# Optimization experiments

Measured on AMD Instinct MI355X. Metric: run time of the kernel, lower is better.

The kernel has to match this reference:

```python
import jax, jax.numpy as jnp
import numpy as np

B = 4096      # batch (tokens)
D_IN = 1024   # input_size_expert
D_HID = 4096  # hidden_size_expert
D_OUT = 1024  # output_size
E = 8         # num_experts


def setup_inputs() -> dict:
    key = jax.random.key(0)
    ks = jax.random.split(key, 9)
    s = lambda fan_in: 1.0 / np.sqrt(fan_in)
    x_expert = jax.random.normal(ks[0], (B, D_IN), dtype=jnp.float32)
    # per-expert weights stacked on leading E axis
    W1 = jax.random.uniform(ks[1], (E, D_IN, D_HID), jnp.float32, -s(D_IN), s(D_IN))
    b1 = jax.random.uniform(ks[2], (E, D_HID), jnp.float32, -s(D_IN), s(D_IN))
    W2 = jax.random.uniform(ks[3], (E, D_HID, D_OUT), jnp.float32, -s(D_HID), s(D_HID))
    b2 = jax.random.uniform(ks[4], (E, D_OUT), jnp.float32, -s(D_HID), s(D_HID))
    # gating network (input_size_gating = input_size_expert, hidden_size_gating = hidden_size_expert)
    Wg1 = jax.random.uniform(ks[5], (D_IN, D_HID), jnp.float32, -s(D_IN), s(D_IN))
    bg1 = jax.random.uniform(ks[6], (D_HID,), jnp.float32, -s(D_IN), s(D_IN))
    Wg2 = jax.random.uniform(ks[7], (D_HID, E), jnp.float32, -s(D_HID), s(D_HID))
    bg2 = jax.random.uniform(ks[8], (E,), jnp.float32, -s(D_HID), s(D_HID))
    return {"x_expert": x_expert, "W1": W1, "b1": b1, "W2": W2, "b2": b2,
            "Wg1": Wg1, "bg1": bg1, "Wg2": Wg2, "bg2": bg2}


def reference(x_expert, W1, b1, W2, b2, Wg1, bg1, Wg2, bg2):
    # gating: MLP + softmax over experts -> [B, E]
    g = jax.nn.relu(x_expert @ Wg1 + bg1)
    gate = jax.nn.softmax(g @ Wg2 + bg2, axis=1)
    # all experts as one batched GEMM: [B, E, D_HID]
    h = jax.nn.relu(jnp.einsum('bi,eih->beh', x_expert, W1) + b1)
    expert_out = jnp.einsum('beh,eho->beo', h, W2) + b2  # [B, E, D_OUT]
    # gate-weighted sum over experts
    return jnp.einsum('be,beo->bo', gate, expert_out)
```

## Files before the change

kernel.cpp:

```cpp
#include <hip/hip_runtime.h>
#include <stdint.h>

typedef __bf16 bf16;
typedef __attribute__((ext_vector_type(8))) __bf16 bf16x8;
typedef __attribute__((ext_vector_type(4))) float f32x4;
typedef unsigned short u16;
typedef unsigned int u32;

#define B_TOK 4096
#define D_IN  1024
#define D_HID 4096
#define D_OUT 1024
#define NE    8
#define KTOT  (NE * D_HID)

#define AS1 __attribute__((address_space(1)))
#define AS3 __attribute__((address_space(3)))

__device__ __forceinline__ u16 f2bf(float f) {
  u32 u = __float_as_uint(f);
  return (u16)((u + 0x7FFFu + ((u >> 16) & 1u)) >> 16);
}
__device__ __forceinline__ u32 pack2(float a, float b) {
  return (u32)f2bf(a) | ((u32)f2bf(b) << 16);
}

__global__ __launch_bounds__(256) void cvt_bf16_kernel(const float* __restrict__ in,
                                                       u32* __restrict__ out, long n) {
  long i = ((long)blockIdx.x * 256 + threadIdx.x) * 8;
  if (i >= n) return;
  const float4* pf = (const float4*)(in + i);
  float4 f0 = pf[0], f1 = pf[1];
  uint4 o = make_uint4(pack2(f0.x, f0.y), pack2(f0.z, f0.w),
                       pack2(f1.x, f1.y), pack2(f1.z, f1.w));
  *(uint4*)(out + i / 2) = o;
}

__global__ __launch_bounds__(256) void transpose_bf16_kernel(const float* __restrict__ in,
                                                             u16* __restrict__ out,
                                                             int R, int C) {
  __shared__ u16 tileT[64][68];
  const size_t bo = (size_t)blockIdx.z * R * C;
  const int c0 = blockIdx.x * 64, r0 = blockIdx.y * 64;
  const int tid = threadIdx.x;
  const int lr = tid >> 4;
  const int lc = (tid & 15) * 4;
#pragma unroll
  for (int p = 0; p < 4; ++p) {
    const int r = p * 16 + lr;
    const float4 v = *(const float4*)(in + bo + (size_t)(r0 + r) * C + c0 + lc);
    tileT[lc + 0][r] = f2bf(v.x);
    tileT[lc + 1][r] = f2bf(v.y);
    tileT[lc + 2][r] = f2bf(v.z);
    tileT[lc + 3][r] = f2bf(v.w);
  }
  __syncthreads();
  const int oc  = tid >> 3;
  const int och = (tid & 7) * 8;
#pragma unroll
  for (int p = 0; p < 2; ++p) {
    const int c = p * 32 + oc;
    bf16x8 v = *(const bf16x8*)(&tileT[c][och]);
    *(bf16x8*)(out + bo + (size_t)(c0 + c) * R + r0 + och) = v;
  }
}

template<int MODE>
__global__ __launch_bounds__(512, 2) void gemm_mfma256(
    const bf16* __restrict__ A,
    const bf16* __restrict__ Bt,
    const float* __restrict__ bias,
    const float* __restrict__ gate,
    void* __restrict__ Cptr,
    int K, long ldB, long kOffB, long ldC, int kIters, int eArg)
{
  __shared__ __align__(16) bf16 smem[65536];

  const int tid  = threadIdx.x;
  const int wave = tid >> 6;
  const int lane = tid & 63;
  const int quad = lane >> 4;
  const int l16  = lane & 15;
  const int wr = (wave >> 2) * 128;
  const int wc = (wave & 3) * 64;

  const int m0 = blockIdx.x * 256;
  const int n0 = blockIdx.y * 256;

  int expert = 0;
  long cColOff = 0;
  const bf16* Bp = Bt;
  const float* biasP = bias;
  if (MODE == 1) {
    if (gridDim.z > 1) { expert = blockIdx.z; cColOff = (long)expert * D_HID; }
    else               { expert = eArg; }
    Bp = Bt + (size_t)expert * D_HID * (size_t)ldB;
    biasP = bias + (size_t)expert * D_HID;
  }
  const int nt = kIters;
  const long kBase = (MODE == 2) ? (long)blockIdx.z * nt * 64 : 0;

  const int sRow = lane >> 3;
  const int sCol = ((lane & 7) ^ sRow) * 8;

  const bf16* aSrc = A  + (size_t)(m0 + wave * 8 + sRow) * K   + kBase + sCol;
  const bf16* bSrc = Bp + (size_t)(n0 + wave * 8 + sRow) * ldB + kOffB + kBase + sCol;
  const int dOff = (wave * 8) * 64;

  f32x4 acc[8][4];
#pragma unroll
  for (int i = 0; i < 8; ++i)
#pragma unroll
    for (int j = 0; j < 4; ++j)
      acc[i][j] = (f32x4){0.f, 0.f, 0.f, 0.f};

#define GLL(tt, bb) do { \
    bf16* dstA = smem + (bb) * 32768 + dOff; \
    bf16* dstB = dstA + 16384; \
    const bf16* srcA = aSrc + (size_t)(tt) * 64; \
    const bf16* srcB = bSrc + (size_t)(tt) * 64; \
    _Pragma("unroll") \
    for (int g_ = 0; g_ < 4; ++g_) { \
      __builtin_amdgcn_global_load_lds((AS1 void*)(srcA + (size_t)g_ * 64 * K), \
                                       (AS3 void*)(dstA + g_ * 64 * 64), 16, 0, 0); \
      __builtin_amdgcn_global_load_lds((AS1 void*)(srcB + (size_t)g_ * 64 * ldB), \
                                       (AS3 void*)(dstB + g_ * 64 * 64), 16, 0, 0); \
    } \
  } while (0)

  GLL(0, 0);

  for (int t = 0; t < nt; ++t) {
    const bf16* Ab = smem + (t & 1) * 32768;
    const bf16* Bb = Ab + 16384;
    asm volatile("s_waitcnt vmcnt(0)" ::: "memory");
    __builtin_amdgcn_s_barrier();
    if (t + 1 < nt) GLL(t + 1, (t + 1) & 1);
#pragma unroll
    for (int kh = 0; kh < 2; ++kh) {
      const int sw = (((kh << 2) + quad) ^ (l16 & 7)) << 3;
      bf16x8 bv[4], av[8];
#pragma unroll
      for (int j = 0; j < 4; ++j)
        bv[j] = *(const bf16x8*)(Bb + (wc + j * 16 + l16) * 64 + sw);
#pragma unroll
      for (int i = 0; i < 8; ++i)
        av[i] = *(const bf16x8*)(Ab + (wr + i * 16 + l16) * 64 + sw);
      __builtin_amdgcn_s_setprio(1);
#pragma unroll
      for (int i = 0; i < 8; ++i)
#pragma unroll
        for (int j = 0; j < 4; ++j)
          acc[i][j] = __builtin_amdgcn_mfma_f32_16x16x32_bf16(av[i], bv[j], acc[i][j], 0, 0, 0);
      __builtin_amdgcn_s_setprio(0);
    }
  }
#undef GLL

  if (MODE <= 1) {
    const int SL = 72;
    u16* slab = (u16*)smem + wave * (16 * SL);
    u16* C = (u16*)Cptr;
    float bv[4];
#pragma unroll
    for (int j = 0; j < 4; ++j) bv[j] = biasP[n0 + wc + j * 16 + l16];
#pragma unroll
    for (int i = 0; i < 8; ++i) {
#pragma unroll
      for (int r = 0; r < 4; ++r) {
        const int lrow = quad * 4 + r;
        float sc = 1.0f;
        if (MODE == 1) sc = gate[(size_t)(m0 + wr + i * 16 + lrow) * NE + expert];
#pragma unroll
        for (int j = 0; j < 4; ++j) {
          float v = fmaxf(acc[i][j][r] + bv[j], 0.0f) * sc;
          slab[lrow * SL + j * 16 + l16] = f2bf(v);
        }
      }
      const int rrow = lane & 15;
      const int c0c  = lane >> 4;
      bf16x8 v0 = *(const bf16x8*)(slab + rrow * SL + c0c * 8);
      bf16x8 v1 = *(const bf16x8*)(slab + rrow * SL + (c0c + 4) * 8);
      u16* orow = C + (size_t)(m0 + wr + i * 16 + rrow) * ldC + cColOff + n0 + wc;
      *(bf16x8*)(orow + c0c * 8)       = v0;
      *(bf16x8*)(orow + (c0c + 4) * 8) = v1;
    }
  } else {
    float* C = (float*)Cptr;
#pragma unroll
    for (int i = 0; i < 8; ++i) {
#pragma unroll
      for (int r = 0; r < 4; ++r) {
        const int row = m0 + wr + i * 16 + quad * 4 + r;
        float* crow = C + (size_t)row * ldC + n0 + wc + l16;
#pragma unroll
        for (int j = 0; j < 4; ++j)
          atomicAdd(crow + j * 16, acc[i][j][r]);
      }
    }
  }
}

__global__ __launch_bounds__(256) void gate_softmax_kernel(const bf16* __restrict__ g,
                                                           const float* __restrict__ Wg2,
                                                           const float* __restrict__ bg2,
                                                           float* __restrict__ gate) {
  const int wave = threadIdx.x >> 6, lane = threadIdx.x & 63;
  const int row = blockIdx.x * 4 + wave;
  const bf16* gr = g + (size_t)row * D_HID;
  float acc[NE];
#pragma unroll
  for (int e = 0; e < NE; ++e) acc[e] = 0.f;
  for (int k = lane; k < D_HID; k += 64) {
    const float gv = (float)gr[k];
    const float* w = Wg2 + (size_t)k * NE;
#pragma unroll
    for (int e = 0; e < NE; ++e) acc[e] += gv * w[e];
  }
#pragma unroll
  for (int e = 0; e < NE; ++e) {
    float v = acc[e];
#pragma unroll
    for (int off = 32; off > 0; off >>= 1) v += __shfl_down(v, off);
    acc[e] = v;
  }
  if (lane == 0) {
    float mx = -3.4e38f;
#pragma unroll
    for (int e = 0; e < NE; ++e) { acc[e] += bg2[e]; mx = fmaxf(mx, acc[e]); }
    float s = 0.f;
#pragma unroll
    for (int e = 0; e < NE; ++e) { acc[e] = __expf(acc[e] - mx); s += acc[e]; }
    const float inv = 1.f / s;
#pragma unroll
    for (int e = 0; e < NE; ++e) gate[(size_t)row * NE + e] = acc[e] * inv;
  }
}

__global__ __launch_bounds__(256) void gate_bias_kernel(const float* __restrict__ gate,
                                                        const float* __restrict__ b2,
                                                        float* __restrict__ out) {
  const int idx = blockIdx.x * 256 + threadIdx.x;
  const int b = idx >> 8;
  const int o = (idx & 255) * 4;
  float4 v = {0.f, 0.f, 0.f, 0.f};
#pragma unroll
  for (int e = 0; e < NE; ++e) {
    const float gv = gate[(size_t)b * NE + e];
    const float4 bb = *(const float4*)(b2 + (size_t)e * D_OUT + o);
    v.x += gv * bb.x; v.y += gv * bb.y; v.z += gv * bb.z; v.w += gv * bb.w;
  }
  *(float4*)(out + (size_t)b * D_OUT + o) = v;
}

extern "C" void kernel_launch(void* const* d_in, const int* in_sizes, int n_in,
                              void* d_out, int out_size, void* d_ws, size_t ws_size,
                              hipStream_t stream) {
  const float* x   = (const float*)d_in[0];
  const float* W1  = (const float*)d_in[1];
  const float* b1  = (const float*)d_in[2];
  const float* W2  = (const float*)d_in[3];
  const float* b2  = (const float*)d_in[4];
  const float* Wg1 = (const float*)d_in[5];
  const float* bg1 = (const float*)d_in[6];
  const float* Wg2 = (const float*)d_in[7];
  const float* bg2 = (const float*)d_in[8];
  float* out = (float*)d_out;

  char* p = (char*)d_ws;
  bf16* xb   = (bf16*)p; p += (size_t)B_TOK * D_IN * 2;
  bf16* Wg1t = (bf16*)p; p += (size_t)D_HID * D_IN * 2;
  bf16* W1t  = (bf16*)p; p += (size_t)NE * D_HID * D_IN * 2;
  bf16* W2t  = (bf16*)p; p += (size_t)D_OUT * KTOT * 2;
  bf16* g    = (bf16*)p; p += (size_t)B_TOK * D_HID * 2;
  float* gate= (float*)p; p += (size_t)B_TOK * NE * 4;
  bf16* hs   = (bf16*)p;
  const size_t fixed = (size_t)(p - (char*)d_ws);
  const bool big = ws_size >= fixed + (size_t)B_TOK * KTOT * 2;

  cvt_bf16_kernel<<<(B_TOK * D_IN / 8 + 255) / 256, 256, 0, stream>>>(x, (u32*)xb, (long)B_TOK * D_IN);
  transpose_bf16_kernel<<<dim3(D_HID / 64, D_IN / 64, 1), 256, 0, stream>>>(Wg1, (u16*)Wg1t, D_IN, D_HID);
  transpose_bf16_kernel<<<dim3(D_HID / 64, D_IN / 64, NE), 256, 0, stream>>>(W1, (u16*)W1t, D_IN, D_HID);
  transpose_bf16_kernel<<<dim3(D_OUT / 64, KTOT / 64, 1), 256, 0, stream>>>(W2, (u16*)W2t, KTOT, D_OUT);
  gemm_mfma256<0><<<dim3(16, 16, 1), 512, 0, stream>>>(xb, Wg1t, bg1, nullptr, g,
                                                       D_IN, (long)D_IN, 0L, (long)D_HID, D_IN / 64, 0);
  gate_softmax_kernel<<<B_TOK / 4, 256, 0, stream>>>(g, Wg2, bg2, gate);
  gate_bias_kernel<<<B_TOK * D_OUT / 4 / 256, 256, 0, stream>>>(gate, b2, out);

  if (big) {
    gemm_mfma256<1><<<dim3(16, 16, NE), 512, 0, stream>>>(xb, W1t, b1, gate, hs,
                                                          D_IN, (long)D_IN, 0L, (long)KTOT, D_IN / 64, 0);
    gemm_mfma256<2><<<dim3(16, 4, 8), 512, 0, stream>>>(hs, W2t, nullptr, nullptr, out,
                                                        KTOT, (long)KTOT, 0L, (long)D_OUT, KTOT / 8 / 64, 0);
  } else {
    for (int e = 0; e < NE; ++e) {
      gemm_mfma256<1><<<dim3(16, 16, 1), 512, 0, stream>>>(xb, W1t, b1, gate, hs,
                                                           D_IN, (long)D_IN, 0L, (long)D_HID, D_IN / 64, e);
      gemm_mfma256<2><<<dim3(16, 4, 2), 512, 0, stream>>>(hs, W2t, nullptr, nullptr, out,
                                                          D_HID, (long)KTOT, (long)e * D_HID, (long)D_OUT,
                                                          D_HID / 2 / 64, e);
    }
  }
}
```

Baseline: 1.006 ms.

## Use 256x128 GEMM tiles with triple-buffered LDS and interleaved prefetch

Shrinks the GEMM block tile from 256x256 to 256x128 and switches from double to triple buffering in LDS, issuing prefetch two tiles ahead. The prefetch loads are split so that half go out before the first MFMA half-step and half after it, with a partial vmcnt wait. Grids are doubled along N, and the split-K factor for the second expert GEMM drops from 8 to 4. This aims at better latency hiding and more blocks in flight, at the cost of lower arithmetic intensity per block and more A-tile reloads.

Result: no change. 1.016 ms (+1.1%).

```diff
diff --git a/kernel.cpp b/kernel.cpp
--- a/kernel.cpp
+++ b/kernel.cpp
@@ -74,7 +74,7 @@
     void* __restrict__ Cptr,
     int K, long ldB, long kOffB, long ldC, int kIters, int eArg)
 {
-  __shared__ __align__(16) bf16 smem[65536];
+  __shared__ __align__(16) bf16 smem[3 * 24576];
 
   const int tid  = threadIdx.x;
   const int wave = tid >> 6;
@@ -82,10 +82,10 @@
   const int quad = lane >> 4;
   const int l16  = lane & 15;
   const int wr = (wave >> 2) * 128;
-  const int wc = (wave & 3) * 64;
+  const int wc = (wave & 3) * 32;
 
   const int m0 = blockIdx.x * 256;
-  const int n0 = blockIdx.y * 256;
+  const int n0 = blockIdx.y * 128;
 
   int expert = 0;
   long cColOff = 0;
@@ -105,65 +105,76 @@
 
   const bf16* aSrc = A  + (size_t)(m0 + wave * 8 + sRow) * K   + kBase + sCol;
   const bf16* bSrc = Bp + (size_t)(n0 + wave * 8 + sRow) * ldB + kOffB + kBase + sCol;
-  const int dOff = (wave * 8) * 64;
-
-  f32x4 acc[8][4];
+
+  f32x4 acc[8][2];
 #pragma unroll
   for (int i = 0; i < 8; ++i)
 #pragma unroll
-    for (int j = 0; j < 4; ++j)
+    for (int j = 0; j < 2; ++j)
       acc[i][j] = (f32x4){0.f, 0.f, 0.f, 0.f};
 
-#define GLL(tt, bb) do { \
-    bf16* dstA = smem + (bb) * 32768 + dOff; \
-    bf16* dstB = dstA + 16384; \
-    const bf16* srcA = aSrc + (size_t)(tt) * 64; \
-    const bf16* srcB = bSrc + (size_t)(tt) * 64; \
-    _Pragma("unroll") \
-    for (int g_ = 0; g_ < 4; ++g_) { \
-      __builtin_amdgcn_global_load_lds((AS1 void*)(srcA + (size_t)g_ * 64 * K), \
-                                       (AS3 void*)(dstA + g_ * 64 * 64), 16, 0, 0); \
-      __builtin_amdgcn_global_load_lds((AS1 void*)(srcB + (size_t)g_ * 64 * ldB), \
-                                       (AS3 void*)(dstB + g_ * 64 * 64), 16, 0, 0); \
+#define GST(tt, bb, s) do { \
+    if ((s) < 4) { \
+      __builtin_amdgcn_global_load_lds( \
+        (AS1 void*)(aSrc + (size_t)(tt) * 64 + (size_t)(s) * 64 * K), \
+        (AS3 void*)(smem + (bb) * 24576 + (s) * 4096 + wave * 512), 16, 0, 0); \
+    } else { \
+      __builtin_amdgcn_global_load_lds( \
+        (AS1 void*)(bSrc + (size_t)(tt) * 64 + (size_t)((s) - 4) * 64 * ldB), \
+        (AS3 void*)(smem + (bb) * 24576 + 16384 + ((s) - 4) * 4096 + wave * 512), 16, 0, 0); \
     } \
   } while (0)
 
-  GLL(0, 0);
-
-  for (int t = 0; t < nt; ++t) {
-    const bf16* Ab = smem + (t & 1) * 32768;
-    const bf16* Bb = Ab + 16384;
-    asm volatile("s_waitcnt vmcnt(0)" ::: "memory");
-    __builtin_amdgcn_s_barrier();
-    if (t + 1 < nt) GLL(t + 1, (t + 1) & 1);
-#pragma unroll
-    for (int kh = 0; kh < 2; ++kh) {
-      const int sw = (((kh << 2) + quad) ^ (l16 & 7)) << 3;
-      bf16x8 bv[4], av[8];
-#pragma unroll
-      for (int j = 0; j < 4; ++j)
-        bv[j] = *(const bf16x8*)(Bb + (wc + j * 16 + l16) * 64 + sw);
-#pragma unroll
-      for (int i = 0; i < 8; ++i)
-        av[i] = *(const bf16x8*)(Ab + (wr + i * 16 + l16) * 64 + sw);
-      __builtin_amdgcn_s_setprio(1);
-#pragma unroll
-      for (int i = 0; i < 8; ++i)
-#pragma unroll
-        for (int j = 0; j < 4; ++j)
-          acc[i][j] = __builtin_amdgcn_mfma_f32_16x16x32_bf16(av[i], bv[j], acc[i][j], 0, 0, 0);
-      __builtin_amdgcn_s_setprio(0);
-    }
-  }
-#undef GLL
+#define TILE_BODY(T, VMW, ISS) do { \
+    const bf16* Ab_ = smem + ((T) % 3) * 24576; \
+    const bf16* Bb_ = Ab_ + 16384; \
+    asm volatile("s_waitcnt vmcnt(" #VMW ")" ::: "memory"); \
+    __builtin_amdgcn_s_barrier(); \
+    __builtin_amdgcn_sched_barrier(0); \
+    if (ISS) { GST((T) + 2, ((T) + 2) % 3, 0); GST((T) + 2, ((T) + 2) % 3, 1); \
+               GST((T) + 2, ((T) + 2) % 3, 2); } \
+    _Pragma("unroll") \
+    for (int kh_ = 0; kh_ < 2; ++kh_) { \
+      const int sw_ = (((kh_ << 2) + quad) ^ (l16 & 7)) << 3; \
+      bf16x8 bv_[2], av_[8]; \
+      _Pragma("unroll") \
+      for (int j_ = 0; j_ < 2; ++j_) \
+        bv_[j_] = *(const bf16x8*)(Bb_ + (wc + j_ * 16 + l16) * 64 + sw_); \
+      _Pragma("unroll") \
+      for (int i_ = 0; i_ < 8; ++i_) \
+        av_[i_] = *(const bf16x8*)(Ab_ + (wr + i_ * 16 + l16) * 64 + sw_); \
+      __builtin_amdgcn_s_setprio(1); \
+      _Pragma("unroll") \
+      for (int i_ = 0; i_ < 8; ++i_) \
+        _Pragma("unroll") \
+        for (int j_ = 0; j_ < 2; ++j_) \
+          acc[i_][j_] = __builtin_amdgcn_mfma_f32_16x16x32_bf16(av_[i_], bv_[j_], acc[i_][j_], 0, 0, 0); \
+      __builtin_amdgcn_s_setprio(0); \
+      if (kh_ == 0 && (ISS)) { GST((T) + 2, ((T) + 2) % 3, 3); \
+                               GST((T) + 2, ((T) + 2) % 3, 4); \
+                               GST((T) + 2, ((T) + 2) % 3, 5); } \
+    } \
+  } while (0)
+
+#pragma unroll
+  for (int s = 0; s < 6; ++s) GST(0, 0, s);
+#pragma unroll
+  for (int s = 0; s < 6; ++s) GST(1, 1, s);
+
+  for (int t = 0; t < nt - 1; ++t) TILE_BODY(t, 6, (t < nt - 2));
+  TILE_BODY(nt - 1, 0, 0);
+
+#undef GST
+#undef TILE_BODY
 
   if (MODE <= 1) {
-    const int SL = 72;
+    const int SL = 40;
     u16* slab = (u16*)smem + wave * (16 * SL);
     u16* C = (u16*)Cptr;
-    float bv[4];
-#pragma unroll
-    for (int j = 0; j < 4; ++j) bv[j] = biasP[n0 + wc + j * 16 + l16];
+    __builtin_amdgcn_s_barrier();
+    float bv[2];
+#pragma unroll
+    for (int j = 0; j < 2; ++j) bv[j] = biasP[n0 + wc + j * 16 + l16];
 #pragma unroll
     for (int i = 0; i < 8; ++i) {
 #pragma unroll
@@ -172,18 +183,16 @@
         float sc = 1.0f;
         if (MODE == 1) sc = gate[(size_t)(m0 + wr + i * 16 + lrow) * NE + expert];
 #pragma unroll
-        for (int j = 0; j < 4; ++j) {
+        for (int j = 0; j < 2; ++j) {
           float v = fmaxf(acc[i][j][r] + bv[j], 0.0f) * sc;
           slab[lrow * SL + j * 16 + l16] = f2bf(v);
         }
       }
       const int rrow = lane & 15;
-      const int c0c  = lane >> 4;
-      bf16x8 v0 = *(const bf16x8*)(slab + rrow * SL + c0c * 8);
-      bf16x8 v1 = *(const bf16x8*)(slab + rrow * SL + (c0c + 4) * 8);
+      const int chk  = lane >> 4;
+      bf16x8 v0 = *(const bf16x8*)(slab + rrow * SL + chk * 8);
       u16* orow = C + (size_t)(m0 + wr + i * 16 + rrow) * ldC + cColOff + n0 + wc;
-      *(bf16x8*)(orow + c0c * 8)       = v0;
-      *(bf16x8*)(orow + (c0c + 4) * 8) = v1;
+      *(bf16x8*)(orow + chk * 8) = v0;
     }
   } else {
     float* C = (float*)Cptr;
@@ -194,7 +203,7 @@
         const int row = m0 + wr + i * 16 + quad * 4 + r;
         float* crow = C + (size_t)row * ldC + n0 + wc + l16;
 #pragma unroll
-        for (int j = 0; j < 4; ++j)
+        for (int j = 0; j < 2; ++j)
           atomicAdd(crow + j * 16, acc[i][j][r]);
       }
     }
@@ -282,21 +291,21 @@
   transpose_bf16_kernel<<<dim3(D_HID / 64, D_IN / 64, 1), 256, 0, stream>>>(Wg1, (u16*)Wg1t, D_IN, D_HID);
   transpose_bf16_kernel<<<dim3(D_HID / 64, D_IN / 64, NE), 256, 0, stream>>>(W1, (u16*)W1t, D_IN, D_HID);
   transpose_bf16_kernel<<<dim3(D_OUT / 64, KTOT / 64, 1), 256, 0, stream>>>(W2, (u16*)W2t, KTOT, D_OUT);
-  gemm_mfma256<0><<<dim3(16, 16, 1), 512, 0, stream>>>(xb, Wg1t, bg1, nullptr, g,
+  gemm_mfma256<0><<<dim3(16, 32, 1), 512, 0, stream>>>(xb, Wg1t, bg1, nullptr, g,
                                                        D_IN, (long)D_IN, 0L, (long)D_HID, D_IN / 64, 0);
   gate_softmax_kernel<<<B_TOK / 4, 256, 0, stream>>>(g, Wg2, bg2, gate);
   gate_bias_kernel<<<B_TOK * D_OUT / 4 / 256, 256, 0, stream>>>(gate, b2, out);
 
   if (big) {
-    gemm_mfma256<1><<<dim3(16, 16, NE), 512, 0, stream>>>(xb, W1t, b1, gate, hs,
+    gemm_mfma256<1><<<dim3(16, 32, NE), 512, 0, stream>>>(xb, W1t, b1, gate, hs,
                                                           D_IN, (long)D_IN, 0L, (long)KTOT, D_IN / 64, 0);
-    gemm_mfma256<2><<<dim3(16, 4, 8), 512, 0, stream>>>(hs, W2t, nullptr, nullptr, out,
-                                                        KTOT, (long)KTOT, 0L, (long)D_OUT, KTOT / 8 / 64, 0);
+    gemm_mfma256<2><<<dim3(16, 8, 4), 512, 0, stream>>>(hs, W2t, nullptr, nullptr, out,
+                                                        KTOT, (long)KTOT, 0L, (long)D_OUT, KTOT / 4 / 64, 0);
   } else {
     for (int e = 0; e < NE; ++e) {
-      gemm_mfma256<1><<<dim3(16, 16, 1), 512, 0, stream>>>(xb, W1t, b1, gate, hs,
+      gemm_mfma256<1><<<dim3(16, 32, 1), 512, 0, stream>>>(xb, W1t, b1, gate, hs,
                                                            D_IN, (long)D_IN, 0L, (long)D_HID, D_IN / 64, e);
-      gemm_mfma256<2><<<dim3(16, 4, 2), 512, 0, stream>>>(hs, W2t, nullptr, nullptr, out,
+      gemm_mfma256<2><<<dim3(16, 8, 2), 512, 0, stream>>>(hs, W2t, nullptr, nullptr, out,
                                                           D_HID, (long)KTOT, (long)e * D_HID, (long)D_OUT,
                                                           D_HID / 2 / 64, e);
     }
```
